# Optimization experiments

Measured on AMD Instinct MI355X. Metric: run time of the kernel, lower is better.

## Reference

```python
import jax, jax.numpy as jnp
import numpy as np

NH = 50000; NO = 50000; E = 500000; D = 256; L = 8; B = 512; C = 117


def setup_inputs() -> dict:
    key = jax.random.key(0)
    ks = jax.random.split(key, 32)
    s = 0.05
    inp = {
        'x_human': jax.random.normal(ks[0], (NH, D), jnp.float32),
        'x_object': jax.random.normal(ks[1], (NO, D), jnp.float32),
        'edge_index_ho': jax.random.randint(ks[2], (2, E), 0, NH),
        'edge_index_oh': jax.random.randint(ks[3], (2, E), 0, NO),
        'edge_attr_ho': jax.random.normal(ks[4], (E, 2), jnp.float32),
        'edge_attr_oh': jax.random.normal(ks[5], (E, 2), jnp.float32),
        'hbatch': jnp.sort(jax.random.randint(ks[6], (NH,), 0, B)),
        'obatch': jnp.sort(jax.random.randint(ks[7], (NO,), 0, B)),
    }
    # GATConv params per relation, stacked over L layers
    names = ['Wsrc', 'Wdst', 'asrc', 'adst', 'Wedge', 'aedge', 'bias']
    shapes = [(L, D, D), (L, D, D), (L, D), (L, D), (L, 2, D), (L, D), (L, D)]
    i = 8
    for rel in ['ho', 'oh']:
        for n, sh in zip(names, shapes):
            inp[f'{n}_{rel}'] = jax.random.normal(ks[i], sh, jnp.float32) * s
            i += 1
    inp['W_emlp'] = jax.random.normal(ks[i], (2, 32), jnp.float32) * s
    inp['b_emlp'] = jnp.zeros((32,), jnp.float32)
    inp['W_p1'] = jax.random.normal(ks[i + 1], (2 * D + 32, C), jnp.float32) * s
    inp['b_p1'] = jnp.zeros((C,), jnp.float32)
    inp['W_p2'] = jax.random.normal(ks[i + 2], (2 * D + 32, C), jnp.float32) * s
    inp['b_p2'] = jnp.zeros((C,), jnp.float32)
    return inp


def _gat(x_src, x_dst, ei, ea, Wsrc, Wdst, asrc, adst, Wedge, aedge, bias, num_dst):
    # PyG GATConv (heads=1, edge_dim=2, add_self_loops=False)
    h_src = x_src @ Wsrc                       # [Ns, D]
    h_dst = x_dst @ Wdst                       # [Nd, D]
    src, dst = ei[0], ei[1]
    a_s = h_src @ asrc                         # [Ns]
    a_d = h_dst @ adst                         # [Nd]
    a_e = (ea @ Wedge) @ aedge                 # [E]
    logit = jax.nn.leaky_relu(a_s[src] + a_d[dst] + a_e, 0.2)
    m = jax.ops.segment_max(logit, dst, num_segments=num_dst)
    ex = jnp.exp(logit - m[dst])
    denom = jax.ops.segment_sum(ex, dst, num_segments=num_dst)
    alpha = ex / denom[dst]                    # segment softmax over dst
    out = jax.ops.segment_sum(h_src[src] * alpha[:, None], dst, num_segments=num_dst)
    return out + bias


def _seg_mean(x, seg, num):
    s = jax.ops.segment_sum(x, seg, num_segments=num)
    cnt = jax.ops.segment_sum(jnp.ones((x.shape[0],), x.dtype), seg, num_segments=num)
    return s / jnp.maximum(cnt, 1.0)[:, None]


def reference(x_human, x_object, edge_index_ho, edge_index_oh, edge_attr_ho,
              edge_attr_oh, hbatch, obatch,
              Wsrc_ho, Wdst_ho, asrc_ho, adst_ho, Wedge_ho, aedge_ho, bias_ho,
              Wsrc_oh, Wdst_oh, asrc_oh, adst_oh, Wedge_oh, aedge_oh, bias_oh,
              W_emlp, b_emlp, W_p1, b_p1, W_p2, b_p2):
    xh, xo = x_human, x_object
    ph, po = None, None
    for l in range(L):
        nxo = _gat(xh, xo, edge_index_ho, edge_attr_ho, Wsrc_ho[l], Wdst_ho[l],
                   asrc_ho[l], adst_ho[l], Wedge_ho[l], aedge_ho[l], bias_ho[l], NO)
        nxh = _gat(xo, xh, edge_index_oh, edge_attr_oh, Wsrc_oh[l], Wdst_oh[l],
                   asrc_oh[l], adst_oh[l], Wedge_oh[l], aedge_oh[l], bias_oh[l], NH)
        nxh = jax.nn.relu(nxh)
        nxo = jax.nn.relu(nxo)
        if ph is not None:
            nxh = nxh + ph
            nxo = nxo + po
        ph, po = nxh, nxo
        xh, xo = nxh, nxo
    hpool = _seg_mean(xh, hbatch, B)           # [B, D]
    opool = _seg_mean(xo, obatch, B)           # [B, D]
    ea = jax.nn.relu(edge_attr_ho @ W_emlp + b_emlp)  # [E, 32]
    edge_batch = hbatch[edge_index_ho[0]]
    epool = _seg_mean(ea, edge_batch, B)       # [B, 32]
    graph_emb = jnp.concatenate([hpool, opool, epool], axis=-1)  # [B, 544]
    l1 = jax.nn.softmax(graph_emb @ W_p1 + b_p1, axis=1)
    l2 = jax.nn.softmax(graph_emb @ W_p2 + b_p2, axis=1)
    return jnp.stack((l1, l2), axis=1)         # [B, 2, C]
```

## Files before the change

kernel.cpp:

```cpp
#include <hip/hip_runtime.h>
#include <math.h>


#define NNODE 50000
#define EDG   500000
#define DIM   256
#define LAY   8
#define BB    512
#define CC    117
#define EMBD  544
#define SCB   49
#define HW    16384
#define HC    16
#define HNW   4
#define LDSE  8192

typedef short bf16x8 __attribute__((ext_vector_type(8)));
typedef float f32x4  __attribute__((ext_vector_type(4)));

static __device__ __forceinline__ float lrelu(float x){ return x >= 0.f ? x : 0.2f*x; }
static __device__ __forceinline__ unsigned short f2b(float f){
  unsigned int u = __float_as_uint(f);
  unsigned int r = (u + 0x7fffu + ((u >> 16) & 1u)) >> 16;
  return (unsigned short)r;
}
static __device__ __forceinline__ float b2f(unsigned short u){
  return __uint_as_float(((unsigned int)u) << 16);
}
static __device__ __forceinline__ float blo(unsigned int u){
  return __uint_as_float(u << 16);
}
static __device__ __forceinline__ float bhi(unsigned int u){
  return __uint_as_float(u & 0xffff0000u);
}
static __device__ __forceinline__ unsigned cvtpk(float lo, float hi){
  unsigned r;
  asm("v_cvt_pk_bf16_f32 %0, %1, %2" : "=v"(r) : "v"(lo), "v"(hi));
  return r;
}
static __device__ __forceinline__ float rdlane_f(float v, int id){
  return __uint_as_float(__builtin_amdgcn_readlane(__float_as_uint(v), id));
}
static __device__ __forceinline__ int rdlane_i(int v, int id){
  return __builtin_amdgcn_readlane(v, id);
}

static __device__ __forceinline__ void gload_lds16(const void* g, void* l){
  __builtin_amdgcn_global_load_lds((const __attribute__((address_space(1))) void*)g,
                                   (__attribute__((address_space(3))) void*)l,
                                   16, 0, 0);
}

__global__ void vcompute_k(const float* __restrict__ Wsho, const float* __restrict__ Wdho,
                           const float* __restrict__ asho, const float* __restrict__ adho,
                           const float* __restrict__ Wsoh, const float* __restrict__ Wdoh,
                           const float* __restrict__ asoh, const float* __restrict__ adoh,
                           float* __restrict__ vbuf){
  int gid = blockIdx.x*blockDim.x + threadIdx.x;
  int wv = gid >> 6, lane = gid & 63;
  if (wv >= 32*DIM) return;
  int p = wv >> 8, k = wv & 255;
  int which = p & 1, rel = (p>>1)&1, l = p>>2;
  const float* W; const float* a;
  if (rel==0){ W = which? Wdho : Wsho; a = which? adho : asho; }
  else       { W = which? Wdoh : Wsoh; a = which? adoh : asoh; }
  W += (size_t)l*DIM*DIM; a += (size_t)l*DIM;
  const float4* w4 = (const float4*)(W + (size_t)k*DIM);
  const float4* a4 = (const float4*)a;
  float4 wv4 = w4[lane], av4 = a4[lane];
  float s = wv4.x*av4.x + wv4.y*av4.y + wv4.z*av4.z + wv4.w*av4.w;
  for (int off=32; off; off>>=1) s += __shfl_xor(s, off);
  if (lane==0) vbuf[(size_t)p*DIM + k] = s;
}

__global__ void wecompute_k(const float* __restrict__ Weho, const float* __restrict__ aeho,
                            const float* __restrict__ Weoh, const float* __restrict__ aeoh,
                            float* __restrict__ webuf){
  int blk = blockIdx.x;
  int rel = blk & 1, l = blk >> 1;
  const float* We = rel? Weoh : Weho;
  const float* ae = rel? aeoh : aeho;
  int lane = threadIdx.x;
  const float4* w0 = (const float4*)(We + (size_t)l*2*DIM);
  const float4* w1 = (const float4*)(We + (size_t)l*2*DIM + DIM);
  const float4* a4 = (const float4*)(ae + (size_t)l*DIM);
  float4 av = a4[lane], x0 = w0[lane], x1 = w1[lane];
  float s0 = x0.x*av.x + x0.y*av.y + x0.z*av.z + x0.w*av.w;
  float s1 = x1.x*av.x + x1.y*av.y + x1.z*av.z + x1.w*av.w;
  for (int off=32; off; off>>=1){ s0 += __shfl_xor(s0, off); s1 += __shfl_xor(s1, off); }
  if (lane==0){ webuf[blk*2] = s0; webuf[blk*2+1] = s1; }
}

__global__ void histp_k(const int* __restrict__ ei_ho, const int* __restrict__ ei_oh,
                        int* __restrict__ phist){
  __shared__ int h[HW];
  int x = blockIdx.x, y = blockIdx.y, z = blockIdx.z, t = threadIdx.x;
  for (int i=t; i<HW; i+=256) h[i] = 0;
  __syncthreads();
  const int* keys = (z==0)? (ei_ho + EDG) : (z==1)? (ei_oh + EDG) : ei_ho;
  int lo = y << 14;
  int e0 = x * (EDG/HC), e1 = e0 + (EDG/HC);
  for (int e = e0 + t; e < e1; e += 256){
    int k = keys[e] - lo;
    if ((unsigned)k < (unsigned)HW) atomicAdd(&h[k], 1);
  }
  __syncthreads();
  int* dst = phist + (size_t)(((z*HNW + y)*HC + x))*HW;
  for (int i=t; i<HW; i+=256) dst[i] = h[i];
}

static __device__ __forceinline__ int4 phist_sum4(const int* __restrict__ phist,
                                                  int z, int idx){
  int win = idx >> 14, off = idx & (HW-1);
  const int* base = phist + (size_t)((z*HNW + win)*HC)*HW + off;
  int4 s = make_int4(0,0,0,0);
  #pragma unroll
  for (int c=0;c<HC;c++){
    int4 v = *(const int4*)(base + (size_t)c*HW);
    s.x += v.x; s.y += v.y; s.z += v.z; s.w += v.w;
  }
  return s;
}

__global__ void scanA_k(const int* __restrict__ phist, int* __restrict__ bsum){
  __shared__ int sh[256];
  int y = blockIdx.y, b = blockIdx.x, t = threadIdx.x;
  int idx = b*1024 + t*4;
  int s = 0;
  if (idx + 3 < NNODE){
    int4 v = phist_sum4(phist, y, idx);
    s = v.x + v.y + v.z + v.w;
  } else {
    for (int j=0;j<4;j++) if (idx+j < NNODE){
      int win = (idx+j) >> 14, off = (idx+j) & (HW-1);
      for (int c=0;c<HC;c++) s += phist[(size_t)((y*HNW+win)*HC+c)*HW + off];
    }
  }
  sh[t] = s; __syncthreads();
  for (int off=128; off; off>>=1){ if (t<off) sh[t] += sh[t+off]; __syncthreads(); }
  if (t==0) bsum[y*SCB + b] = sh[0];
}

__global__ void scanB_k(int* __restrict__ bsum, int* __restrict__ boff,
                        int* __restrict__ rp0, int* __restrict__ rp1, int* __restrict__ rp2){
  int t = threadIdx.x;
  if (t >= 3) return;
  int run = 0;
  for (int i=0;i<SCB;i++){ boff[t*SCB+i] = run; run += bsum[t*SCB+i]; }
  int* rp = (t==0)? rp0 : (t==1)? rp1 : rp2;
  rp[NNODE] = run;
}

__global__ void scanC_k(const int* __restrict__ phist, const int* __restrict__ boff,
                        int* __restrict__ rp0, int* __restrict__ rp1, int* __restrict__ rp2){
  __shared__ int sh[256];
  int y = blockIdx.y, b = blockIdx.x, t = threadIdx.x;
  int* rp = (y==0)? rp0 : (y==1)? rp1 : rp2;
  int idx = b*1024 + t*4;
  int c[4] = {0,0,0,0};
  if (idx + 3 < NNODE){
    int4 v = phist_sum4(phist, y, idx);
    c[0]=v.x; c[1]=v.y; c[2]=v.z; c[3]=v.w;
  } else {
    for (int j=0;j<4;j++) if (idx+j < NNODE){
      int win = (idx+j) >> 14, off = (idx+j) & (HW-1);
      for (int cc=0;cc<HC;cc++) c[j] += phist[(size_t)((y*HNW+win)*HC+cc)*HW + off];
    }
  }
  int mysum = c[0]+c[1]+c[2]+c[3];
  sh[t] = mysum; __syncthreads();
  for (int off=1; off<256; off<<=1){
    int v = (t>=off) ? sh[t-off] : 0;
    __syncthreads();
    sh[t] += v;
    __syncthreads();
  }
  int base = boff[y*SCB + b] + (sh[t] - mysum);
  int run = 0;
  for (int j=0;j<4;j++){
    if (idx+j < NNODE) rp[idx+j] = base + run;
    run += c[j];
  }
}

__global__ void scatter3_k(const int* __restrict__ ei_ho, const int* __restrict__ ei_oh,
                           const float* __restrict__ ea_ho, const float* __restrict__ ea_oh,
                           const int* __restrict__ rp0, const int* __restrict__ rp1,
                           const int* __restrict__ rp2, int* __restrict__ cur,
                           float4* __restrict__ rec0, float4* __restrict__ rec1,
                           float2* __restrict__ eap2){
  int e = blockIdx.x*blockDim.x + threadIdx.x;
  if (e >= EDG) return;
  int y = blockIdx.y;
  if (y == 0){
    int d = ei_ho[EDG + e];
    int pos = rp0[d] + atomicAdd(&cur[d], 1);
    rec0[pos] = make_float4(__int_as_float(ei_ho[e]), ea_ho[2*e], ea_ho[2*e+1],
                            __int_as_float(d));
  } else if (y == 1){
    int d = ei_oh[EDG + e];
    int pos = rp1[d] + atomicAdd(&cur[NNODE + d], 1);
    rec1[pos] = make_float4(__int_as_float(ei_oh[e]), ea_oh[2*e], ea_oh[2*e+1],
                            __int_as_float(d));
  } else {
    int s = ei_ho[e];
    int pos = rp2[s] + atomicAdd(&cur[2*NNODE + s], 1);
    eap2[pos] = make_float2(ea_ho[2*e], ea_ho[2*e+1]);
  }
}

__global__ void xcdg_k(const float* __restrict__ xh_in, const float* __restrict__ xo_in,
                       unsigned short* __restrict__ xhb, unsigned short* __restrict__ xob,
                       const float* __restrict__ vbuf, float* __restrict__ aset){
  int gid = blockIdx.x*blockDim.x + threadIdx.x;
  int w = gid >> 6, lane = gid & 63;
  if (w >= NNODE) return;
  int z = blockIdx.y;
  const float* X = z? xo_in : xh_in;
  unsigned short* O = z? xob : xhb;
  const float* v1 = vbuf + (size_t)(z? 2:0)*DIM;
  const float* v2 = vbuf + (size_t)(z? 1:3)*DIM;
  float* o1 = aset + (size_t)(z? 2:0)*NNODE;
  float* o2 = aset + (size_t)(z? 1:3)*NNODE;
  float4 xv = ((const float4*)(X + (size_t)w*DIM))[lane];
  uint2 ob; ob.x = cvtpk(xv.x, xv.y); ob.y = cvtpk(xv.z, xv.w);
  ((uint2*)O)[(size_t)w*64 + lane] = ob;
  float4 a = ((const float4*)v1)[lane];
  float4 b = ((const float4*)v2)[lane];
  float s1 = xv.x*a.x + xv.y*a.y + xv.z*a.z + xv.w*a.w;
  float s2 = xv.x*b.x + xv.y*b.y + xv.z*b.z + xv.w*b.w;
  for (int off=32; off; off>>=1){ s1 += __shfl_xor(s1, off); s2 += __shfl_xor(s2, off); }
  if (lane==0){ o1[w] = s1; o2[w] = s2; }
}

__global__ void wtconv_k(const float* __restrict__ Who, const float* __restrict__ Woh,
                         unsigned short* __restrict__ Wt){
  int gid = blockIdx.x*blockDim.x + threadIdx.x;
  int rel = gid >> 19;
  int rem = gid & ((1<<19)-1);
  int l = rem >> 16;
  int idx = rem & 65535;
  int n = idx >> 8, k = idx & 255;
  const float* W = rel ? Woh : Who;
  Wt[gid] = f2b(W[(size_t)l*65536 + (size_t)k*256 + n]);
}

__global__ __launch_bounds__(256) void gemmb2_k(const unsigned short* __restrict__ A0,
                                                const unsigned short* __restrict__ A1,
                                                const unsigned short* __restrict__ B0,
                                                const unsigned short* __restrict__ B1,
                                                unsigned short* __restrict__ H0,
                                                unsigned short* __restrict__ H1, int M){
  __shared__ __align__(16) unsigned short As[4096];
  __shared__ __align__(16) unsigned short Bs[4096];
  int z = blockIdx.z;
  const unsigned short* A  = z? A1 : A0;
  const unsigned short* Bt = z? B1 : B0;
  unsigned short* H        = z? H1 : H0;
  int tid = threadIdx.x;
  int col0 = blockIdx.x * 128;
  int row0 = blockIdx.y * 128;
  int w = tid >> 6, lane = tid & 63;
  int q = lane >> 4, ml = lane & 15;
  f32x4 acc[2][8];
  #pragma unroll
  for (int i=0;i<2;i++)
    #pragma unroll
    for (int j=0;j<8;j++) acc[i][j] = (f32x4){0.f,0.f,0.f,0.f};

  const unsigned short* srcA[2];
  const unsigned short* srcB[2];
  #pragma unroll
  for (int p=0;p<2;p++){
    int c = p*256 + w*64 + lane;
    int row = ((c>>6)<<4) | (c&15);
    int sq  = (c>>4)&3;
    int gr = row0 + row; if (gr >= M) gr = M-1;
    srcA[p] = A  + (size_t)gr*256 + sq*8;
    srcB[p] = Bt + (size_t)(col0 + row)*256 + sq*8;
  }

  for (int k0 = 0; k0 < 256; k0 += 32){
    #pragma unroll
    for (int p = 0; p < 2; ++p){
      gload_lds16(srcA[p], &As[(size_t)(p*256 + w*64)*8]);
      gload_lds16(srcB[p], &Bs[(size_t)(p*256 + w*64)*8]);
      srcA[p] += 32; srcB[p] += 32;
    }
    __syncthreads();
    bf16x8 a0 = *(const bf16x8*)&As[(((2*w+0)*4 + q)*16 + ml)*8];
    bf16x8 a1 = *(const bf16x8*)&As[(((2*w+1)*4 + q)*16 + ml)*8];
    #pragma unroll
    for (int nf = 0; nf < 8; ++nf){
      bf16x8 b = *(const bf16x8*)&Bs[((nf*4 + q)*16 + ml)*8];
      acc[0][nf] = __builtin_amdgcn_mfma_f32_16x16x32_bf16(a0, b, acc[0][nf], 0,0,0);
      acc[1][nf] = __builtin_amdgcn_mfma_f32_16x16x32_bf16(a1, b, acc[1][nf], 0,0,0);
    }
    __syncthreads();
  }
  #pragma unroll
  for (int mf = 0; mf < 2; ++mf){
    #pragma unroll
    for (int r = 0; r < 4; ++r){
      int gr = row0 + 32*w + 16*mf + q*4 + r;
      if (gr < M){
        #pragma unroll
        for (int nf = 0; nf < 8; ++nf)
          H[(size_t)gr*256 + col0 + nf*16 + ml] = f2b(acc[mf][nf][r]);
      }
    }
  }
}

__global__ __launch_bounds__(256) void elsm_k(
    const int* __restrict__ rp0, const float4* __restrict__ rec0,
    const int* __restrict__ rp1, const float4* __restrict__ rec1,
    const float* __restrict__ cur_a, const float* __restrict__ wepl,
    uint2* __restrict__ lgsrc0, uint2* __restrict__ lgsrc1,
    float2* __restrict__ ms0, float2* __restrict__ ms1){
  __shared__ float lgs[LDSE];
  int rel = blockIdx.y;
  const int* rp = rel? rp1 : rp0;
  const float4* rec = rel? rec1 : rec0;
  const float* a_s = cur_a + (size_t)(rel? 2:0)*NNODE;
  const float* a_d = cur_a + (size_t)(rel? 3:1)*NNODE;
  float w0 = wepl[rel? 2:0], w1 = wepl[rel? 3:1];
  uint2* lgsrc = rel? lgsrc1 : lgsrc0;
  float2* ms = rel? ms1 : ms0;
  int n0 = blockIdx.x * 128;
  int n1 = n0 + 128; if (n1 > NNODE) n1 = NNODE;
  int t = threadIdx.x;
  int e0 = rp[n0], e1 = rp[n1];
  bool fit = (e1 - e0) <= LDSE;
  for (int e = e0 + t; e < e1; e += 256){
    float4 r = rec[e];
    int src = __float_as_int(r.x);
    int dst = __float_as_int(r.w);
    float lg = lrelu(a_s[src] + a_d[dst] + r.y*w0 + r.z*w1);
    lgsrc[e] = make_uint2(__float_as_uint(lg), (unsigned)src);
    if (fit) lgs[e - e0] = lg;
  }
  __syncthreads();
  if (t < 128){
    int n = n0 + t;
    if (n < NNODE){
      int st = rp[n], en = rp[n+1];
      float m = -INFINITY, s = 0.f;
      if (fit){
        for (int p=st;p<en;p++) m = fmaxf(m, lgs[p-e0]);
        for (int p=st;p<en;p++) s += __expf(lgs[p-e0] - m);
      } else {
        for (int p=st;p<en;p++) m = fmaxf(m, __uint_as_float(lgsrc[p].x));
        for (int p=st;p<en;p++) s += __expf(__uint_as_float(lgsrc[p].x) - m);
      }
      ms[n] = make_float2(m, __builtin_amdgcn_rcpf(s));
    }
  }
}

__global__ void attn2_k(const int* __restrict__ rp0, const uint2* __restrict__ lgsrc0,
                        const int* __restrict__ rp1, const uint2* __restrict__ lgsrc1,
                        const float2* __restrict__ ms0, const float2* __restrict__ ms1,
                        float* __restrict__ nxt_a,
                        const unsigned short* __restrict__ hs0,
                        const unsigned short* __restrict__ hs1,
                        const float* __restrict__ bias0, const float* __restrict__ bias1,
                        const unsigned short* __restrict__ xprev0,
                        const unsigned short* __restrict__ xprev1,
                        unsigned short* __restrict__ xnext0,
                        unsigned short* __restrict__ xnext1,
                        const float* __restrict__ vbl,
                        int hasRes, int doNext){
  int gid = blockIdx.x*blockDim.x + threadIdx.x;
  int w = gid >> 6, lane = gid & 63;
  if (w >= NNODE) return;
  int rel = blockIdx.y;
  const int* rowptr = rel? rp1 : rp0;
  const uint2* lgsrc = rel? lgsrc1 : lgsrc0;
  const float2* msb = rel? ms1 : ms0;
  const unsigned short* hs = rel? hs1 : hs0;
  const float* bias = rel? bias1 : bias0;
  const unsigned short* xprev = rel? xprev1 : xprev0;
  unsigned short* xnext = rel? xnext1 : xnext0;

  int st = rowptr[w], en = rowptr[w+1];
  int deg = en - st;
  float2 msv = msb[w];

  float4 bv = ((const float4*)bias)[lane];
  uint2 rres = ((const uint2*)xprev)[(size_t)w*64 + lane];
  float4 va = ((const float4*)(vbl + (size_t)(rel? 0:2)*DIM))[lane];
  float4 vc = ((const float4*)(vbl + (size_t)(rel? 3:1)*DIM))[lane];

  float ax=0.f, ay=0.f, az=0.f, aw=0.f;
  if (deg > 0 && deg <= 64){
    int sreg = 0; float wgt = 0.f;
    if (lane < deg){
      uint2 ls = lgsrc[st + lane];
      sreg = (int)ls.y;
      wgt = __expf(__uint_as_float(ls.x) - msv.x) * msv.y;
    }
    int i = 0;
    for (; i + 7 < deg; i += 8){
      float wi[8]; const uint2* rp[8];
      #pragma unroll
      for (int j=0;j<8;j++){
        wi[j] = rdlane_f(wgt, i+j);
        rp[j] = (const uint2*)(hs + (size_t)rdlane_i(sreg, i+j)*DIM);
      }
      uint2 hv[8];
      #pragma unroll
      for (int j=0;j<8;j++) hv[j] = rp[j][lane];
      #pragma unroll
      for (int j=0;j<8;j++){
        ax += wi[j]*blo(hv[j].x); ay += wi[j]*bhi(hv[j].x);
        az += wi[j]*blo(hv[j].y); aw += wi[j]*bhi(hv[j].y);
      }
    }
    for (; i + 3 < deg; i += 4){
      float wi[4]; const uint2* rp[4];
      #pragma unroll
      for (int j=0;j<4;j++){
        wi[j] = rdlane_f(wgt, i+j);
        rp[j] = (const uint2*)(hs + (size_t)rdlane_i(sreg, i+j)*DIM);
      }
      uint2 hv[4];
      #pragma unroll
      for (int j=0;j<4;j++) hv[j] = rp[j][lane];
      #pragma unroll
      for (int j=0;j<4;j++){
        ax += wi[j]*blo(hv[j].x); ay += wi[j]*bhi(hv[j].x);
        az += wi[j]*blo(hv[j].y); aw += wi[j]*bhi(hv[j].y);
      }
    }
    for (; i < deg; ++i){
      float wi = rdlane_f(wgt, i);
      const uint2* rp = (const uint2*)(hs + (size_t)rdlane_i(sreg, i)*DIM);
      uint2 hv = rp[lane];
      ax += wi*blo(hv.x); ay += wi*bhi(hv.x);
      az += wi*blo(hv.y); aw += wi*bhi(hv.y);
    }
  } else if (deg > 64){
    for (int p = st; p < en; ++p){
      uint2 ls = lgsrc[p];
      float wgt = __expf(__uint_as_float(ls.x) - msv.x) * msv.y;
      const uint2* rp = (const uint2*)(hs + (size_t)ls.y*DIM);
      uint2 hv = rp[lane];
      ax += wgt*blo(hv.x); ay += wgt*bhi(hv.x);
      az += wgt*blo(hv.y); aw += wgt*bhi(hv.y);
    }
  }

  float resw = hasRes ? 1.f : 0.f;
  float4 o;
  o.x = fmaxf(ax + bv.x, 0.f) + resw*blo(rres.x);
  o.y = fmaxf(ay + bv.y, 0.f) + resw*bhi(rres.x);
  o.z = fmaxf(az + bv.z, 0.f) + resw*blo(rres.y);
  o.w = fmaxf(aw + bv.w, 0.f) + resw*bhi(rres.y);
  uint2 ob; ob.x = cvtpk(o.x, o.y); ob.y = cvtpk(o.z, o.w);
  ((uint2*)xnext)[(size_t)w*64 + lane] = ob;
  if (doNext){
    float s1 = o.x*va.x + o.y*va.y + o.z*va.z + o.w*va.w;
    float s2 = o.x*vc.x + o.y*vc.y + o.z*vc.z + o.w*vc.w;
    for (int off=32; off; off>>=1){ s1 += __shfl_xor(s1, off); s2 += __shfl_xor(s2, off); }
    if (lane==0){
      float* asn = nxt_a + (size_t)(rel? 0:2)*NNODE;
      float* adn = nxt_a + (size_t)(rel? 3:1)*NNODE;
      asn[w] = s1; adn[w] = s2;
    }
  }
}

__device__ __forceinline__ int lowerb(const int* a, int n, int v){
  int lo=0, hi=n;
  while (lo < hi){ int m = (lo+hi)>>1; if (a[m] < v) lo = m+1; else hi = m; }
  return lo;
}

__global__ void pool2_k(const unsigned short* __restrict__ xh, const unsigned short* __restrict__ xo,
                        const int* __restrict__ hbatch, const int* __restrict__ obatch,
                        float* __restrict__ hpool, float* __restrict__ opool){
  int z = blockIdx.y;
  const unsigned short* x = z? xo : xh;
  const int* batch = z? obatch : hbatch;
  float* out = z? opool : hpool;
  int b = blockIdx.x, t = threadIdx.x;
  int st = lowerb(batch, NNODE, b), en = lowerb(batch, NNODE, b+1);
  float s = 0.f;
  for (int i=st;i<en;i++) s += b2f(x[(size_t)i*DIM + t]);
  out[(size_t)b*DIM + t] = s / fmaxf((float)(en - st), 1.f);
}

__global__ void epool_k(const int* __restrict__ rp_src, const int* __restrict__ hbatch,
                        const float2* __restrict__ eaperm, const float* __restrict__ Wem,
                        const float* __restrict__ bem, float* __restrict__ epool){
  __shared__ float ps[8][33];
  int b = blockIdx.x, t = threadIdx.x;
  int j = t & 31, g = t >> 5;
  int nst = lowerb(hbatch, NNODE, b), nen = lowerb(hbatch, NNODE, b+1);
  int est = rp_src[nst], een = rp_src[nen];
  float w0 = Wem[j], w1 = Wem[32+j], bb = bem[j];
  float s = 0.f;
  for (int p = est + g; p < een; p += 8){
    float2 e = eaperm[p];
    s += fmaxf(e.x*w0 + e.y*w1 + bb, 0.f);
  }
  ps[g][j] = s; __syncthreads();
  if (g == 0){
    float tot = 0.f;
    #pragma unroll
    for (int gg=0; gg<8; gg++) tot += ps[gg][j];
    epool[(size_t)b*32 + j] = tot / fmaxf((float)(een - est), 1.f);
  }
}

__global__ void head_k(const float* __restrict__ hpool, const float* __restrict__ opool,
                       const float* __restrict__ epool,
                       const float* __restrict__ Wp1, const float* __restrict__ bp1,
                       const float* __restrict__ Wp2, const float* __restrict__ bp2,
                       float* __restrict__ out){
  __shared__ float emb[EMBD];
  __shared__ float red[256];
  int b = blockIdx.x, t = threadIdx.x;
  emb[t] = hpool[(size_t)b*DIM + t];
  emb[DIM + t] = opool[(size_t)b*DIM + t];
  if (t < 32) emb[2*DIM + t] = epool[(size_t)b*32 + t];
  __syncthreads();
  for (int h = 0; h < 2; ++h){
    const float* Wp = h? Wp2 : Wp1;
    const float* bp = h? bp2 : bp1;
    float logit = -INFINITY;
    if (t < CC){
      float s = bp[t];
      for (int k=0;k<EMBD;k++) s += emb[k]*Wp[(size_t)k*CC + t];
      logit = s;
    }
    red[t] = logit; __syncthreads();
    for (int off=128; off; off>>=1){ if (t<off) red[t] = fmaxf(red[t], red[t+off]); __syncthreads(); }
    float mx = red[0]; __syncthreads();
    float ex = (t < CC) ? expf(logit - mx) : 0.f;
    red[t] = ex; __syncthreads();
    for (int off=128; off; off>>=1){ if (t<off) red[t] += red[t+off]; __syncthreads(); }
    float sm = red[0]; __syncthreads();
    if (t < CC) out[((size_t)b*2 + h)*CC + t] = ex / sm;
  }
}

extern "C" void kernel_launch(void* const* d_in, const int* in_sizes, int n_in,
                              void* d_out, int out_size, void* d_ws, size_t ws_size,
                              hipStream_t stream) {
  (void)in_sizes; (void)n_in; (void)out_size; (void)ws_size;
  const float* xh_in   = (const float*)d_in[0];
  const float* xo_in   = (const float*)d_in[1];
  const int*   ei_ho   = (const int*)d_in[2];
  const int*   ei_oh   = (const int*)d_in[3];
  const float* ea_ho   = (const float*)d_in[4];
  const float* ea_oh   = (const float*)d_in[5];
  const int*   hbatch  = (const int*)d_in[6];
  const int*   obatch  = (const int*)d_in[7];
  const float* Wsrc_ho = (const float*)d_in[8];
  const float* Wdst_ho = (const float*)d_in[9];
  const float* asrc_ho = (const float*)d_in[10];
  const float* adst_ho = (const float*)d_in[11];
  const float* Wedge_ho= (const float*)d_in[12];
  const float* aedge_ho= (const float*)d_in[13];
  const float* bias_ho = (const float*)d_in[14];
  const float* Wsrc_oh = (const float*)d_in[15];
  const float* Wdst_oh = (const float*)d_in[16];
  const float* asrc_oh = (const float*)d_in[17];
  const float* adst_oh = (const float*)d_in[18];
  const float* Wedge_oh= (const float*)d_in[19];
  const float* aedge_oh= (const float*)d_in[20];
  const float* bias_oh = (const float*)d_in[21];
  const float* W_emlp  = (const float*)d_in[22];
  const float* b_emlp  = (const float*)d_in[23];
  const float* W_p1    = (const float*)d_in[24];
  const float* b_p1    = (const float*)d_in[25];
  const float* W_p2    = (const float*)d_in[26];
  const float* b_p2    = (const float*)d_in[27];
  float* out = (float*)d_out;

  size_t ND = (size_t)NNODE*DIM;
  float* f = (float*)d_ws;
  float* aset0 = f;
  float* aset1 = aset0 + 4*NNODE;
  float* vbuf  = aset1 + 4*NNODE;
  float* webuf = vbuf + 32*DIM;
  float* hpool = webuf + 32;
  float* opool = hpool + (size_t)BB*DIM;
  float* epool = opool + (size_t)BB*DIM;
  float4* rec_ho  = (float4*)(epool + (size_t)BB*32);
  float4* rec_oh  = rec_ho + EDG;
  float2* eap_src = (float2*)(rec_oh + EDG);
  unsigned short* xhb0 = (unsigned short*)(eap_src + EDG);
  unsigned short* xhb1 = xhb0 + ND;
  unsigned short* xob0 = xhb1 + ND;
  unsigned short* xob1 = xob0 + ND;
  unsigned short* hSb0 = xob1 + ND;
  unsigned short* hSb1 = hSb0 + ND;
  unsigned short* Wtb  = hSb1 + ND;
  int* cur     = (int*)(Wtb + (size_t)2*LAY*DIM*DIM);
  int* rp_ho   = cur + 3*NNODE;
  int* rp_oh   = rp_ho + NNODE + 1;
  int* rp_src  = rp_oh + NNODE + 1;
  int* bsum    = rp_src + NNODE + 1;
  int* boff    = bsum + 3*SCB;
  int* phist   = boff + 3*SCB;
  uint2*  lgsrc_ho = (uint2*)phist;
  uint2*  lgsrc_oh = lgsrc_ho + EDG;
  float2* msb_ho   = (float2*)(lgsrc_oh + EDG);
  float2* msb_oh   = msb_ho + NNODE;

  hipMemsetAsync(cur, 0, sizeof(int)*3*NNODE, stream);
  vcompute_k<<<2048, 256, 0, stream>>>(Wsrc_ho, Wdst_ho, asrc_ho, adst_ho,
                                       Wsrc_oh, Wdst_oh, asrc_oh, adst_oh, vbuf);
  wecompute_k<<<16, 64, 0, stream>>>(Wedge_ho, aedge_ho, Wedge_oh, aedge_oh, webuf);
  wtconv_k<<<4096, 256, 0, stream>>>(Wsrc_ho, Wsrc_oh, Wtb);
  histp_k<<<dim3(HC, HNW, 3), 256, 0, stream>>>(ei_ho, ei_oh, phist);
  scanA_k<<<dim3(SCB, 3), 256, 0, stream>>>(phist, bsum);
  scanB_k<<<1, 64, 0, stream>>>(bsum, boff, rp_ho, rp_oh, rp_src);
  scanC_k<<<dim3(SCB, 3), 256, 0, stream>>>(phist, boff, rp_ho, rp_oh, rp_src);
  scatter3_k<<<dim3(1954, 3), 256, 0, stream>>>(ei_ho, ei_oh, ea_ho, ea_oh,
                                                rp_ho, rp_oh, rp_src, cur,
                                                rec_ho, rec_oh, eap_src);
  xcdg_k<<<dim3(12500, 2), 256, 0, stream>>>(xh_in, xo_in, xhb1, xob1, vbuf, aset0);

  const unsigned short* xh = xhb1;
  const unsigned short* xo = xob1;
  unsigned short* xh_bufs[2] = {xhb0, xhb1};
  unsigned short* xo_bufs[2] = {xob0, xob1};
  float* asets[2] = {aset0, aset1};
  for (int l = 0; l < LAY; ++l){
    unsigned short* xo_n = xo_bufs[l & 1];
    unsigned short* xh_n = xh_bufs[l & 1];
    float* cur_a = asets[l & 1];
    float* nxt_a = asets[(l & 1) ^ 1];
    int doNext = (l < LAY-1);
    int ln = doNext ? (l+1) : l;
    elsm_k<<<dim3(391, 2), 256, 0, stream>>>(rp_ho, rec_ho, rp_oh, rec_oh,
                                             cur_a, webuf + (size_t)l*4,
                                             lgsrc_ho, lgsrc_oh, msb_ho, msb_oh);
    gemmb2_k<<<dim3(2, 391, 2), 256, 0, stream>>>(xh, xo,
                                                  Wtb + (size_t)l*DIM*DIM,
                                                  Wtb + (size_t)(LAY + l)*DIM*DIM,
                                                  hSb0, hSb1, NNODE);
    attn2_k<<<dim3(12500, 2), 256, 0, stream>>>(rp_ho, lgsrc_ho,
                                                rp_oh, lgsrc_oh,
                                                msb_ho, msb_oh,
                                                nxt_a,
                                                hSb0, hSb1,
                                                bias_ho + (size_t)l*DIM, bias_oh + (size_t)l*DIM,
                                                xo, xh, xo_n, xh_n,
                                                vbuf + (size_t)ln*4*DIM,
                                                l > 0, doNext);
    xh = xh_n; xo = xo_n;
  }

  pool2_k<<<dim3(BB, 2), 256, 0, stream>>>(xh, xo, hbatch, obatch, hpool, opool);
  epool_k<<<BB, 256, 0, stream>>>(rp_src, hbatch, eap_src, W_emlp, b_emlp, epool);
  head_k<<<BB, 256, 0, stream>>>(hpool, opool, epool, W_p1, b_p1, W_p2, b_p2, out);
}
```

Measured before the change: 1.505 ms.

## Merge edge-softmax into GEMM launch and store normalized attention weights

The per-layer edge-logit/softmax kernel and the bf16 GEMM now run as one launch: a third z-slice of blocks handles the softmax and shares LDS through a union, with LDSE halved to fit. The softmax kernel writes the final normalized alpha into lgsrc, so attn2_k no longer reads max/sum and recomputes exp. The setup scatter and the bf16-convert kernels are merged into one launch. This cuts launches and per-edge exp work in the aggregation step, at the cost of an extra write pass over edges and more blocks falling back to the slower non-LDS path because the LDS buffer is smaller.

```diff
diff --git a/kernel.cpp b/kernel.cpp
--- a/kernel.cpp
+++ b/kernel.cpp
@@ -13,7 +13,7 @@
 #define HW    16384
 #define HC    16
 #define HNW   4
-#define LDSE  8192
+#define LDSE  4096
 
 typedef short bf16x8 __attribute__((ext_vector_type(8)));
 typedef float f32x4  __attribute__((ext_vector_type(4)));
@@ -183,54 +183,56 @@
   }
 }
 
-__global__ void scatter3_k(const int* __restrict__ ei_ho, const int* __restrict__ ei_oh,
-                           const float* __restrict__ ea_ho, const float* __restrict__ ea_oh,
-                           const int* __restrict__ rp0, const int* __restrict__ rp1,
-                           const int* __restrict__ rp2, int* __restrict__ cur,
-                           float4* __restrict__ rec0, float4* __restrict__ rec1,
-                           float2* __restrict__ eap2){
-  int e = blockIdx.x*blockDim.x + threadIdx.x;
-  if (e >= EDG) return;
+__global__ void sxc_k(const float* __restrict__ xh_in, const float* __restrict__ xo_in,
+                      unsigned short* __restrict__ xhb, unsigned short* __restrict__ xob,
+                      const float* __restrict__ vbuf, float* __restrict__ aset,
+                      const int* __restrict__ ei_ho, const int* __restrict__ ei_oh,
+                      const float* __restrict__ ea_ho, const float* __restrict__ ea_oh,
+                      const int* __restrict__ rp0, const int* __restrict__ rp1,
+                      const int* __restrict__ rp2, int* __restrict__ cur,
+                      float4* __restrict__ rec0, float4* __restrict__ rec1,
+                      float2* __restrict__ eap2){
   int y = blockIdx.y;
-  if (y == 0){
-    int d = ei_ho[EDG + e];
-    int pos = rp0[d] + atomicAdd(&cur[d], 1);
-    rec0[pos] = make_float4(__int_as_float(ei_ho[e]), ea_ho[2*e], ea_ho[2*e+1],
-                            __int_as_float(d));
-  } else if (y == 1){
-    int d = ei_oh[EDG + e];
-    int pos = rp1[d] + atomicAdd(&cur[NNODE + d], 1);
-    rec1[pos] = make_float4(__int_as_float(ei_oh[e]), ea_oh[2*e], ea_oh[2*e+1],
-                            __int_as_float(d));
+  if (y < 2){
+    int gid = blockIdx.x*blockDim.x + threadIdx.x;
+    int w = gid >> 6, lane = gid & 63;
+    if (w >= NNODE) return;
+    int z = y;
+    const float* X = z? xo_in : xh_in;
+    unsigned short* O = z? xob : xhb;
+    const float* v1 = vbuf + (size_t)(z? 2:0)*DIM;
+    const float* v2 = vbuf + (size_t)(z? 1:3)*DIM;
+    float* o1 = aset + (size_t)(z? 2:0)*NNODE;
+    float* o2 = aset + (size_t)(z? 1:3)*NNODE;
+    float4 xv = ((const float4*)(X + (size_t)w*DIM))[lane];
+    uint2 ob; ob.x = cvtpk(xv.x, xv.y); ob.y = cvtpk(xv.z, xv.w);
+    ((uint2*)O)[(size_t)w*64 + lane] = ob;
+    float4 a = ((const float4*)v1)[lane];
+    float4 b = ((const float4*)v2)[lane];
+    float s1 = xv.x*a.x + xv.y*a.y + xv.z*a.z + xv.w*a.w;
+    float s2 = xv.x*b.x + xv.y*b.y + xv.z*b.z + xv.w*b.w;
+    for (int off=32; off; off>>=1){ s1 += __shfl_xor(s1, off); s2 += __shfl_xor(s2, off); }
+    if (lane==0){ o1[w] = s1; o2[w] = s2; }
   } else {
-    int s = ei_ho[e];
-    int pos = rp2[s] + atomicAdd(&cur[2*NNODE + s], 1);
-    eap2[pos] = make_float2(ea_ho[2*e], ea_ho[2*e+1]);
-  }
-}
-
-__global__ void xcdg_k(const float* __restrict__ xh_in, const float* __restrict__ xo_in,
-                       unsigned short* __restrict__ xhb, unsigned short* __restrict__ xob,
-                       const float* __restrict__ vbuf, float* __restrict__ aset){
-  int gid = blockIdx.x*blockDim.x + threadIdx.x;
-  int w = gid >> 6, lane = gid & 63;
-  if (w >= NNODE) return;
-  int z = blockIdx.y;
-  const float* X = z? xo_in : xh_in;
-  unsigned short* O = z? xob : xhb;
-  const float* v1 = vbuf + (size_t)(z? 2:0)*DIM;
-  const float* v2 = vbuf + (size_t)(z? 1:3)*DIM;
-  float* o1 = aset + (size_t)(z? 2:0)*NNODE;
-  float* o2 = aset + (size_t)(z? 1:3)*NNODE;
-  float4 xv = ((const float4*)(X + (size_t)w*DIM))[lane];
-  uint2 ob; ob.x = cvtpk(xv.x, xv.y); ob.y = cvtpk(xv.z, xv.w);
-  ((uint2*)O)[(size_t)w*64 + lane] = ob;
-  float4 a = ((const float4*)v1)[lane];
-  float4 b = ((const float4*)v2)[lane];
-  float s1 = xv.x*a.x + xv.y*a.y + xv.z*a.z + xv.w*a.w;
-  float s2 = xv.x*b.x + xv.y*b.y + xv.z*b.z + xv.w*b.w;
-  for (int off=32; off; off>>=1){ s1 += __shfl_xor(s1, off); s2 += __shfl_xor(s2, off); }
-  if (lane==0){ o1[w] = s1; o2[w] = s2; }
+    int e = blockIdx.x*blockDim.x + threadIdx.x;
+    if (e >= EDG) return;
+    int yy = y - 2;
+    if (yy == 0){
+      int d = ei_ho[EDG + e];
+      int pos = rp0[d] + atomicAdd(&cur[d], 1);
+      rec0[pos] = make_float4(__int_as_float(ei_ho[e]), ea_ho[2*e], ea_ho[2*e+1],
+                              __int_as_float(d));
+    } else if (yy == 1){
+      int d = ei_oh[EDG + e];
+      int pos = rp1[d] + atomicAdd(&cur[NNODE + d], 1);
+      rec1[pos] = make_float4(__int_as_float(ei_oh[e]), ea_oh[2*e], ea_oh[2*e+1],
+                              __int_as_float(d));
+    } else {
+      int s = ei_ho[e];
+      int pos = rp2[s] + atomicAdd(&cur[2*NNODE + s], 1);
+      eap2[pos] = make_float2(ea_ho[2*e], ea_ho[2*e+1]);
+    }
+  }
 }
 
 __global__ void wtconv_k(const float* __restrict__ Who, const float* __restrict__ Woh,
@@ -245,122 +247,125 @@
   Wt[gid] = f2b(W[(size_t)l*65536 + (size_t)k*256 + n]);
 }
 
-__global__ __launch_bounds__(256) void gemmb2_k(const unsigned short* __restrict__ A0,
-                                                const unsigned short* __restrict__ A1,
-                                                const unsigned short* __restrict__ B0,
-                                                const unsigned short* __restrict__ B1,
-                                                unsigned short* __restrict__ H0,
-                                                unsigned short* __restrict__ H1, int M){
-  __shared__ __align__(16) unsigned short As[4096];
-  __shared__ __align__(16) unsigned short Bs[4096];
-  int z = blockIdx.z;
-  const unsigned short* A  = z? A1 : A0;
-  const unsigned short* Bt = z? B1 : B0;
-  unsigned short* H        = z? H1 : H0;
-  int tid = threadIdx.x;
-  int col0 = blockIdx.x * 128;
-  int row0 = blockIdx.y * 128;
-  int w = tid >> 6, lane = tid & 63;
-  int q = lane >> 4, ml = lane & 15;
-  f32x4 acc[2][8];
-  #pragma unroll
-  for (int i=0;i<2;i++)
-    #pragma unroll
-    for (int j=0;j<8;j++) acc[i][j] = (f32x4){0.f,0.f,0.f,0.f};
-
-  const unsigned short* srcA[2];
-  const unsigned short* srcB[2];
-  #pragma unroll
-  for (int p=0;p<2;p++){
-    int c = p*256 + w*64 + lane;
-    int row = ((c>>6)<<4) | (c&15);
-    int sq  = (c>>4)&3;
-    int gr = row0 + row; if (gr >= M) gr = M-1;
-    srcA[p] = A  + (size_t)gr*256 + sq*8;
-    srcB[p] = Bt + (size_t)(col0 + row)*256 + sq*8;
-  }
-
-  for (int k0 = 0; k0 < 256; k0 += 32){
-    #pragma unroll
-    for (int p = 0; p < 2; ++p){
-      gload_lds16(srcA[p], &As[(size_t)(p*256 + w*64)*8]);
-      gload_lds16(srcB[p], &Bs[(size_t)(p*256 + w*64)*8]);
-      srcA[p] += 32; srcB[p] += 32;
-    }
-    __syncthreads();
-    bf16x8 a0 = *(const bf16x8*)&As[(((2*w+0)*4 + q)*16 + ml)*8];
-    bf16x8 a1 = *(const bf16x8*)&As[(((2*w+1)*4 + q)*16 + ml)*8];
-    #pragma unroll
-    for (int nf = 0; nf < 8; ++nf){
-      bf16x8 b = *(const bf16x8*)&Bs[((nf*4 + q)*16 + ml)*8];
-      acc[0][nf] = __builtin_amdgcn_mfma_f32_16x16x32_bf16(a0, b, acc[0][nf], 0,0,0);
-      acc[1][nf] = __builtin_amdgcn_mfma_f32_16x16x32_bf16(a1, b, acc[1][nf], 0,0,0);
-    }
-    __syncthreads();
-  }
-  #pragma unroll
-  for (int mf = 0; mf < 2; ++mf){
-    #pragma unroll
-    for (int r = 0; r < 4; ++r){
-      int gr = row0 + 32*w + 16*mf + q*4 + r;
-      if (gr < M){
-        #pragma unroll
-        for (int nf = 0; nf < 8; ++nf)
-          H[(size_t)gr*256 + col0 + nf*16 + ml] = f2b(acc[mf][nf][r]);
-      }
-    }
-  }
-}
-
-__global__ __launch_bounds__(256) void elsm_k(
+__global__ __launch_bounds__(256) void gesm_k(
+    const unsigned short* __restrict__ A0, const unsigned short* __restrict__ A1,
+    const unsigned short* __restrict__ B0, const unsigned short* __restrict__ B1,
+    unsigned short* __restrict__ H0, unsigned short* __restrict__ H1, int M,
     const int* __restrict__ rp0, const float4* __restrict__ rec0,
     const int* __restrict__ rp1, const float4* __restrict__ rec1,
     const float* __restrict__ cur_a, const float* __restrict__ wepl,
-    uint2* __restrict__ lgsrc0, uint2* __restrict__ lgsrc1,
-    float2* __restrict__ ms0, float2* __restrict__ ms1){
-  __shared__ float lgs[LDSE];
-  int rel = blockIdx.y;
-  const int* rp = rel? rp1 : rp0;
-  const float4* rec = rel? rec1 : rec0;
-  const float* a_s = cur_a + (size_t)(rel? 2:0)*NNODE;
-  const float* a_d = cur_a + (size_t)(rel? 3:1)*NNODE;
-  float w0 = wepl[rel? 2:0], w1 = wepl[rel? 3:1];
-  uint2* lgsrc = rel? lgsrc1 : lgsrc0;
-  float2* ms = rel? ms1 : ms0;
-  int n0 = blockIdx.x * 128;
-  int n1 = n0 + 128; if (n1 > NNODE) n1 = NNODE;
-  int t = threadIdx.x;
-  int e0 = rp[n0], e1 = rp[n1];
-  bool fit = (e1 - e0) <= LDSE;
-  for (int e = e0 + t; e < e1; e += 256){
-    float4 r = rec[e];
-    int src = __float_as_int(r.x);
-    int dst = __float_as_int(r.w);
-    float lg = lrelu(a_s[src] + a_d[dst] + r.y*w0 + r.z*w1);
-    lgsrc[e] = make_uint2(__float_as_uint(lg), (unsigned)src);
-    if (fit) lgs[e - e0] = lg;
-  }
-  __syncthreads();
-  if (t < 128){
-    int n = n0 + t;
-    if (n < NNODE){
-      int st = rp[n], en = rp[n+1];
-      float m = -INFINITY, s = 0.f;
-      if (fit){
-        for (int p=st;p<en;p++) m = fmaxf(m, lgs[p-e0]);
-        for (int p=st;p<en;p++) s += __expf(lgs[p-e0] - m);
-      } else {
-        for (int p=st;p<en;p++) m = fmaxf(m, __uint_as_float(lgsrc[p].x));
-        for (int p=st;p<en;p++) s += __expf(__uint_as_float(lgsrc[p].x) - m);
-      }
-      ms[n] = make_float2(m, __builtin_amdgcn_rcpf(s));
+    uint2* __restrict__ lgsrc0, uint2* __restrict__ lgsrc1){
+  union SMu {
+    struct { unsigned short As[4096]; unsigned short Bs[4096]; } g;
+    float lgs[LDSE];
+  };
+  __shared__ __align__(16) SMu sh;
+
+  if (blockIdx.z < 2){
+    int z = blockIdx.z;
+    const unsigned short* A  = z? A1 : A0;
+    const unsigned short* Bt = z? B1 : B0;
+    unsigned short* H        = z? H1 : H0;
+    int tid = threadIdx.x;
+    int col0 = blockIdx.x * 128;
+    int row0 = blockIdx.y * 128;
+    int w = tid >> 6, lane = tid & 63;
+    int q = lane >> 4, ml = lane & 15;
+    f32x4 acc[2][8];
+    #pragma unroll
+    for (int i=0;i<2;i++)
+      #pragma unroll
+      for (int j=0;j<8;j++) acc[i][j] = (f32x4){0.f,0.f,0.f,0.f};
+
+    const unsigned short* srcA[2];
+    const unsigned short* srcB[2];
+    #pragma unroll
+    for (int p=0;p<2;p++){
+      int c = p*256 + w*64 + lane;
+      int row = ((c>>6)<<4) | (c&15);
+      int sq  = (c>>4)&3;
+      int gr = row0 + row; if (gr >= M) gr = M-1;
+      srcA[p] = A  + (size_t)gr*256 + sq*8;
+      srcB[p] = Bt + (size_t)(col0 + row)*256 + sq*8;
+    }
+
+    for (int k0 = 0; k0 < 256; k0 += 32){
+      #pragma unroll
+      for (int p = 0; p < 2; ++p){
+        gload_lds16(srcA[p], &sh.g.As[(size_t)(p*256 + w*64)*8]);
+        gload_lds16(srcB[p], &sh.g.Bs[(size_t)(p*256 + w*64)*8]);
+        srcA[p] += 32; srcB[p] += 32;
+      }
+      __syncthreads();
+      bf16x8 a0 = *(const bf16x8*)&sh.g.As[(((2*w+0)*4 + q)*16 + ml)*8];
+      bf16x8 a1 = *(const bf16x8*)&sh.g.As[(((2*w+1)*4 + q)*16 + ml)*8];
+      #pragma unroll
+      for (int nf = 0; nf < 8; ++nf){
+        bf16x8 b = *(const bf16x8*)&sh.g.Bs[((nf*4 + q)*16 + ml)*8];
+        acc[0][nf] = __builtin_amdgcn_mfma_f32_16x16x32_bf16(a0, b, acc[0][nf], 0,0,0);
+        acc[1][nf] = __builtin_amdgcn_mfma_f32_16x16x32_bf16(a1, b, acc[1][nf], 0,0,0);
+      }
+      __syncthreads();
+    }
+    #pragma unroll
+    for (int mf = 0; mf < 2; ++mf){
+      #pragma unroll
+      for (int r = 0; r < 4; ++r){
+        int gr = row0 + 32*w + 16*mf + q*4 + r;
+        if (gr < M){
+          #pragma unroll
+          for (int nf = 0; nf < 8; ++nf)
+            H[(size_t)gr*256 + col0 + nf*16 + ml] = f2b(acc[mf][nf][r]);
+        }
+      }
+    }
+  } else {
+    int rel = blockIdx.x;
+    const int* rp = rel? rp1 : rp0;
+    const float4* rec = rel? rec1 : rec0;
+    const float* a_s = cur_a + (size_t)(rel? 2:0)*NNODE;
+    const float* a_d = cur_a + (size_t)(rel? 3:1)*NNODE;
+    float w0 = wepl[rel? 2:0], w1 = wepl[rel? 3:1];
+    uint2* lgsrc = rel? lgsrc1 : lgsrc0;
+    int n0 = blockIdx.y * 128;
+    int n1 = n0 + 128; if (n1 > NNODE) n1 = NNODE;
+    int t = threadIdx.x;
+    int e0 = rp[n0], e1 = rp[n1];
+    bool fit = (e1 - e0) <= LDSE;
+    for (int e = e0 + t; e < e1; e += 256){
+      float4 r = rec[e];
+      int src = __float_as_int(r.x);
+      int dst = __float_as_int(r.w);
+      float lg = lrelu(a_s[src] + a_d[dst] + r.y*w0 + r.z*w1);
+      lgsrc[e] = make_uint2(__float_as_uint(lg), (unsigned)src);
+      if (fit) sh.lgs[e - e0] = lg;
+    }
+    __syncthreads();
+    if (t < 128){
+      int n = n0 + t;
+      if (n < NNODE){
+        int st = rp[n], en = rp[n+1];
+        float m = -INFINITY, s = 0.f;
+        if (fit){
+          for (int p=st;p<en;p++) m = fmaxf(m, sh.lgs[p-e0]);
+          for (int p=st;p<en;p++) s += __expf(sh.lgs[p-e0] - m);
+          float inv = __builtin_amdgcn_rcpf(s);
+          for (int p=st;p<en;p++)
+            lgsrc[p].x = __float_as_uint(__expf(sh.lgs[p-e0] - m) * inv);
+        } else {
+          for (int p=st;p<en;p++) m = fmaxf(m, __uint_as_float(lgsrc[p].x));
+          for (int p=st;p<en;p++) s += __expf(__uint_as_float(lgsrc[p].x) - m);
+          float inv = __builtin_amdgcn_rcpf(s);
+          for (int p=st;p<en;p++)
+            lgsrc[p].x = __float_as_uint(__expf(__uint_as_float(lgsrc[p].x) - m) * inv);
+        }
+      }
     }
   }
 }
 
 __global__ void attn2_k(const int* __restrict__ rp0, const uint2* __restrict__ lgsrc0,
                         const int* __restrict__ rp1, const uint2* __restrict__ lgsrc1,
-                        const float2* __restrict__ ms0, const float2* __restrict__ ms1,
                         float* __restrict__ nxt_a,
                         const unsigned short* __restrict__ hs0,
                         const unsigned short* __restrict__ hs1,
@@ -377,7 +382,6 @@
   int rel = blockIdx.y;
   const int* rowptr = rel? rp1 : rp0;
   const uint2* lgsrc = rel? lgsrc1 : lgsrc0;
-  const float2* msb = rel? ms1 : ms0;
   const unsigned short* hs = rel? hs1 : hs0;
   const float* bias = rel? bias1 : bias0;
   const unsigned short* xprev = rel? xprev1 : xprev0;
@@ -385,7 +389,6 @@
 
   int st = rowptr[w], en = rowptr[w+1];
   int deg = en - st;
-  float2 msv = msb[w];
 
   float4 bv = ((const float4*)bias)[lane];
   uint2 rres = ((const uint2*)xprev)[(size_t)w*64 + lane];
@@ -398,7 +401,7 @@
     if (lane < deg){
       uint2 ls = lgsrc[st + lane];
       sreg = (int)ls.y;
-      wgt = __expf(__uint_as_float(ls.x) - msv.x) * msv.y;
+      wgt = __uint_as_float(ls.x);
     }
     int i = 0;
     for (; i + 7 < deg; i += 8){
@@ -443,7 +446,7 @@
   } else if (deg > 64){
     for (int p = st; p < en; ++p){
       uint2 ls = lgsrc[p];
-      float wgt = __expf(__uint_as_float(ls.x) - msv.x) * msv.y;
+      float wgt = __uint_as_float(ls.x);
       const uint2* rp = (const uint2*)(hs + (size_t)ls.y*DIM);
       uint2 hv = rp[lane];
       ax += wgt*blo(hv.x); ay += wgt*bhi(hv.x);
@@ -608,8 +611,6 @@
   int* phist   = boff + 3*SCB;
   uint2*  lgsrc_ho = (uint2*)phist;
   uint2*  lgsrc_oh = lgsrc_ho + EDG;
-  float2* msb_ho   = (float2*)(lgsrc_oh + EDG);
-  float2* msb_oh   = msb_ho + NNODE;
 
   hipMemsetAsync(cur, 0, sizeof(int)*3*NNODE, stream);
   vcompute_k<<<2048, 256, 0, stream>>>(Wsrc_ho, Wdst_ho, asrc_ho, adst_ho,
@@ -620,10 +621,10 @@
   scanA_k<<<dim3(SCB, 3), 256, 0, stream>>>(phist, bsum);
   scanB_k<<<1, 64, 0, stream>>>(bsum, boff, rp_ho, rp_oh, rp_src);
   scanC_k<<<dim3(SCB, 3), 256, 0, stream>>>(phist, boff, rp_ho, rp_oh, rp_src);
-  scatter3_k<<<dim3(1954, 3), 256, 0, stream>>>(ei_ho, ei_oh, ea_ho, ea_oh,
-                                                rp_ho, rp_oh, rp_src, cur,
-                                                rec_ho, rec_oh, eap_src);
-  xcdg_k<<<dim3(12500, 2), 256, 0, stream>>>(xh_in, xo_in, xhb1, xob1, vbuf, aset0);
+  sxc_k<<<dim3(12500, 5), 256, 0, stream>>>(xh_in, xo_in, xhb1, xob1, vbuf, aset0,
+                                            ei_ho, ei_oh, ea_ho, ea_oh,
+                                            rp_ho, rp_oh, rp_src, cur,
+                                            rec_ho, rec_oh, eap_src);
 
   const unsigned short* xh = xhb1;
   const unsigned short* xo = xob1;
@@ -637,16 +638,15 @@
     float* nxt_a = asets[(l & 1) ^ 1];
     int doNext = (l < LAY-1);
     int ln = doNext ? (l+1) : l;
-    elsm_k<<<dim3(391, 2), 256, 0, stream>>>(rp_ho, rec_ho, rp_oh, rec_oh,
-                                             cur_a, webuf + (size_t)l*4,
-                                             lgsrc_ho, lgsrc_oh, msb_ho, msb_oh);
-    gemmb2_k<<<dim3(2, 391, 2), 256, 0, stream>>>(xh, xo,
-                                                  Wtb + (size_t)l*DIM*DIM,
-                                                  Wtb + (size_t)(LAY + l)*DIM*DIM,
-                                                  hSb0, hSb1, NNODE);
+    gesm_k<<<dim3(2, 391, 3), 256, 0, stream>>>(xh, xo,
+                                                Wtb + (size_t)l*DIM*DIM,
+                                                Wtb + (size_t)(LAY + l)*DIM*DIM,
+                                                hSb0, hSb1, NNODE,
+                                                rp_ho, rec_ho, rp_oh, rec_oh,
+                                                cur_a, webuf + (size_t)l*4,
+                                                lgsrc_ho, lgsrc_oh);
     attn2_k<<<dim3(12500, 2), 256, 0, stream>>>(rp_ho, lgsrc_ho,
                                                 rp_oh, lgsrc_oh,
-                                                msb_ho, msb_oh,
                                                 nxt_a,
                                                 hSb0, hSb1,
                                                 bias_ho + (size_t)l*DIM, bias_oh + (size_t)l*DIM,
```

Measured after the change: 1.462 ms. 1.03x faster.
